# Kernel tuning notes

Measured on AMD Instinct MI355X. Metric: run time of the kernel, lower is better.

The kernel has to match this reference:

```python
import jax, jax.numpy as jnp
import numpy as np

H, W = 256, 256
FRONT_K = 8
ALPHA_T = 1.0 / 255.0
EPS = 1e-8               # transmittance early-stop threshold (meta_f32[4])
BG = (0.0, 0.0, 0.0)     # background color
CHUNK = 128              # gaussians composited per scan step


def setup_inputs() -> dict:
    key = jax.random.key(0)
    k1, k2, k3, k4, k5, k6, k7 = jax.random.split(key, 7)
    B, G = 2, 8192
    # gaussian centers spread over the image plane
    means2d = jax.random.uniform(k1, (B, G, 2), jnp.float32) * jnp.array([W, H], jnp.float32)
    # positive-definite conics (inverse 2D covariance): a, c > 0, |b| < sqrt(a*c)
    a = 0.05 + 0.45 * jax.random.uniform(k2, (B, G), jnp.float32)
    c = 0.05 + 0.45 * jax.random.uniform(k3, (B, G), jnp.float32)
    b = 0.5 * (jax.random.uniform(k4, (B, G), jnp.float32) - 0.5) * jnp.sqrt(a * c)
    conics = jnp.stack([a, b, c], axis=-1)
    colors = jax.random.uniform(k5, (B, G, 3), jnp.float32)
    opacities = jax.random.uniform(k6, (B, G), jnp.float32)
    depths = jax.random.uniform(k7, (B, G), jnp.float32) * 10.0
    return {"means2d": means2d, "conics": conics, "colors": colors,
            "opacities": opacities, "depths": depths}


def _rasterize_one(means2d, conics, colors, opacities, depths):
    # depth sort (stable, front-to-back)
    perm = jnp.argsort(depths, stable=True)
    m = means2d[perm]      # [G,2]
    co = conics[perm]      # [G,3]
    col = colors[perm]     # [G,3]
    op = opacities[perm]   # [G]
    G = m.shape[0]
    n_chunks = G // CHUNK

    px = jnp.arange(W, dtype=jnp.float32) + 0.5  # pixel centers
    py = jnp.arange(H, dtype=jnp.float32) + 0.5
    bg = jnp.asarray(BG, jnp.float32)

    def step(carry, chunk):
        accum, T, count = carry                    # [H,W,3], [H,W], [H,W] int32
        mC, coC, colC, opC = chunk                 # [K,2],[K,3],[K,3],[K]
        dx = px[None, None, :] - mC[:, 0][:, None, None]   # [K,1,W]
        dy = py[None, :, None] - mC[:, 1][:, None, None]   # [K,H,1]
        a = coC[:, 0][:, None, None]
        b = coC[:, 1][:, None, None]
        c = coC[:, 2][:, None, None]
        sigma = 0.5 * (a * dx * dx + c * dy * dy) + b * dx * dy  # [K,H,W]
        alpha = jnp.minimum(opC[:, None, None] * jnp.exp(-sigma), 0.999)
        alpha = jnp.where((sigma >= 0.0) & (alpha >= ALPHA_T), alpha, 0.0)
        kept = (alpha > 0.0).astype(jnp.int32)
        # front_k: only the first FRONT_K contributing gaussians per pixel
        before = count[None] + jnp.cumsum(kept, axis=0) - kept
        alpha = jnp.where(before < FRONT_K, alpha, 0.0)
        kept = (alpha > 0.0).astype(jnp.int32)
        one_m = 1.0 - alpha
        cp = jnp.cumprod(one_m, axis=0)                              # [K,H,W]
        Tc = T[None] * jnp.concatenate([jnp.ones((1, H, W), alpha.dtype), cp[:-1]], 0)
        w = jnp.where(Tc > EPS, Tc * alpha, 0.0)                     # early-stop gate
        accum = accum + jnp.einsum('khw,kc->hwc', w, colC)
        T = T * cp[-1]
        count = count + jnp.sum(kept, axis=0)
        return (accum, T, count), None

    chunks = (m.reshape(n_chunks, CHUNK, 2),
              co.reshape(n_chunks, CHUNK, 3),
              col.reshape(n_chunks, CHUNK, 3),
              op.reshape(n_chunks, CHUNK))
    init = (jnp.zeros((H, W, 3), jnp.float32),
            jnp.ones((H, W), jnp.float32),
            jnp.zeros((H, W), jnp.int32))
    (accum, T, _), _ = jax.lax.scan(step, init, chunks)
    return accum + T[..., None] * bg


def reference(means2d, conics, colors, opacities, depths):
    return jax.vmap(_rasterize_one)(means2d, conics, colors, opacities, depths)
```

## Files before the change

### kernel.cpp

```cpp
#include <hip/hip_runtime.h>
#include <math.h>

#define GN 8192
#define BN 2
#define HN 256
#define WN 256
#define FRONT_K 8
#define EPS_T 1e-8f
#define ALPHA_T (1.0f / 255.0f)
#define TDIM 32
#define NTILE (TDIM * TDIM)
#define CAP 256

__global__ __launch_bounds__(64) void pgr_clear(unsigned* __restrict__ cur)
{
    cur[blockIdx.x * 64 + threadIdx.x] = 0u;
}

__global__ __launch_bounds__(64) void pgr_prep(
    const float* __restrict__ means2d, const float* __restrict__ conics,
    const float* __restrict__ colors, const float* __restrict__ opac,
    const float* __restrict__ depths,
    float4* __restrict__ dat0, float4* __restrict__ dat1,
    float* __restrict__ dat2, unsigned long long* __restrict__ kdat,
    unsigned* __restrict__ cur, unsigned* __restrict__ ent)
{
    const int p = threadIdx.x >> 3;
    const int q = threadIdx.x & 7;
    int g = blockIdx.x * 8 + p;
    int b = g >> 13, i = g & (GN - 1);
    float2 mxy = reinterpret_cast<const float2*>(means2d)[g];
    float mx = mxy.x, my = mxy.y;
    float ca = conics[3 * g], cb = conics[3 * g + 1], cc = conics[3 * g + 2];
    float r = colors[3 * g], g2 = colors[3 * g + 1], b3 = colors[3 * g + 2];
    float op = opac[g];
    float dep = depths[g];

    if (q == 0) {
        dat0[g] = make_float4(mx, my, ca, cb);
        dat1[g] = make_float4(cc, op, r, g2);
        dat2[g] = b3;
        kdat[g] = ((unsigned long long)__float_as_uint(dep) << 13) | (unsigned)i;
    }

    float s = (op > 0.f) ? (__logf(255.0f * op) + 1e-4f) : -1.0f;
    if (s < 0.f) return;
    float det = fmaxf(ca * cc - cb * cb, 1e-12f);
    float dxm = sqrtf(2.f * s * cc / det) + 0.02f;
    float dym = sqrtf(2.f * s * ca / det) + 0.02f;
    int x0 = (int)floorf(mx - dxm - 0.5f), x1 = (int)ceilf(mx + dxm - 0.5f);
    int y0 = (int)floorf(my - dym - 0.5f), y1 = (int)ceilf(my + dym - 0.5f);
    if (x1 < 0 || x0 > WN - 1 || y1 < 0 || y0 > HN - 1) return;
    x0 = max(x0, 0); x1 = min(x1, WN - 1);
    y0 = max(y0, 0); y1 = min(y1, HN - 1);
    int tx0 = x0 >> 3, tx1 = x1 >> 3, ty0 = y0 >> 3, ty1 = y1 >> 3;
    int nx = tx1 - tx0 + 1;
    int ntl = nx * (ty1 - ty0 + 1);

    for (int idx = q; idx < ntl; idx += 8) {
        int ty = idx / nx;
        int tx = idx - ty * nx;
        int t = b * NTILE + (ty0 + ty) * TDIM + (tx0 + tx);
        unsigned pos = atomicAdd(&cur[t], 1u);
        if (pos < CAP) ent[t * CAP + (int)pos] = (unsigned)i;
    }
}

__device__ __forceinline__ int rank_of(const unsigned long long* s_key,
                                       unsigned long long k, int L)
{
    int rank = 0, j = 0;
    for (; j + 4 <= L; j += 4) {
        unsigned long long k0 = s_key[j], k1 = s_key[j + 1];
        unsigned long long k2 = s_key[j + 2], k3 = s_key[j + 3];
        rank += (int)(k0 < k) + (int)(k1 < k) + (int)(k2 < k) + (int)(k3 < k);
    }
    for (; j < L; ++j) rank += (int)(s_key[j] < k);
    return rank;
}

__global__ __launch_bounds__(256) void pgr_raster(
    const float4* __restrict__ dat0, const float4* __restrict__ dat1,
    const float* __restrict__ dat2, const unsigned long long* __restrict__ kdat,
    const unsigned* __restrict__ cur, const unsigned* __restrict__ ent,
    float* __restrict__ out)
{
    const int b = blockIdx.z;
    const int t = b * NTILE + blockIdx.y * TDIM + blockIdx.x;
    const int tid = threadIdx.x;
    const int tx0 = blockIdx.x * 8, ty0 = blockIdx.y * 8;
    const int bG = b * GN;

    __shared__ unsigned long long s_key[CAP];
    __shared__ float4 s_d0[CAP], s_d1[CAP];
    __shared__ float s_d2[CAP];

    const int base = t * CAP;
    const int L = min((int)cur[t], CAP);

    unsigned long long myk = 0;
    float4 r0, r1;
    float r2 = 0.f;
    if (tid < L) {
        int idx = bG + (int)ent[base + tid];
        myk = kdat[idx];
        r0 = dat0[idx];
        r1 = dat1[idx];
        r2 = dat2[idx];
        s_key[tid] = myk;
    }
    __syncthreads();

    if (tid < L) {
        int rank = rank_of(s_key, myk, L);
        s_d0[rank] = r0; s_d1[rank] = r1; s_d2[rank] = r2;
    }
    __syncthreads();

    if (tid >= 64) return;

    const int lx = tid & 7, ly = tid >> 3;
    const float px = tx0 + lx + 0.5f, py = ty0 + ly + 0.5f;

    float accR = 0.f, accG = 0.f, accB = 0.f, T = 1.f;
    int count = 0;
    bool done = false;

    for (int i0 = 0; i0 < L; i0 += 8) {
        if (__all((int)done)) break;
        float alpha[8], colR[8], colG[8], colB[8];
        bool valid[8];
        #pragma unroll
        for (int k = 0; k < 8; ++k) {
            int idx = i0 + k;
            bool act = (idx < L) && !done;
            int ii = act ? idx : i0;
            float4 d0 = s_d0[ii];
            float4 d1 = s_d1[ii];
            float dx = __fsub_rn(px, d0.x);
            float dy = __fsub_rn(py, d0.y);
            float t1 = __fmul_rn(__fmul_rn(d0.z, dx), dx);
            float t2 = __fmul_rn(__fmul_rn(d1.x, dy), dy);
            float sigma = __fadd_rn(__fmul_rn(0.5f, __fadd_rn(t1, t2)),
                                    __fmul_rn(__fmul_rn(d0.w, dx), dy));
            bool v = act && sigma >= 0.f && sigma <= 5.55f;
            float al = v ? fminf(__fmul_rn(d1.y, __expf(-sigma)), 0.999f) : 0.f;
            valid[k] = v && (al >= ALPHA_T);
            alpha[k] = al;
            colR[k] = d1.z; colG[k] = d1.w; colB[k] = s_d2[ii];
        }
        #pragma unroll
        for (int k = 0; k < 8; ++k) {
            if (valid[k] && !done) {
                float al = alpha[k];
                if (T > EPS_T) {
                    float w = __fmul_rn(T, al);
                    accR += w * colR[k];
                    accG += w * colG[k];
                    accB += w * colB[k];
                }
                T = __fmul_rn(T, __fsub_rn(1.f, al));
                count++;
                if (count >= FRONT_K || T <= EPS_T) done = true;
            }
        }
    }

    int o = ((b * HN + (ty0 + ly)) * WN + (tx0 + lx)) * 3;
    out[o] = accR;
    out[o + 1] = accG;
    out[o + 2] = accB;
}

extern "C" void kernel_launch(void* const* d_in, const int* in_sizes, int n_in,
                              void* d_out, int out_size, void* d_ws, size_t ws_size,
                              hipStream_t stream) {
    const float* means2d = (const float*)d_in[0];
    const float* conics  = (const float*)d_in[1];
    const float* colors  = (const float*)d_in[2];
    const float* opac    = (const float*)d_in[3];
    const float* depths  = (const float*)d_in[4];
    float* out = (float*)d_out;

    const int BG = BN * GN;
    float4*             dat0 = (float4*)d_ws;
    float4*             dat1 = dat0 + BG;
    float*              dat2 = (float*)(dat1 + BG);
    unsigned long long* kdat = (unsigned long long*)(dat2 + BG);
    unsigned*           cur  = (unsigned*)(kdat + BG);
    unsigned*           ent  = cur + BN * NTILE;

    pgr_clear<<<(BN * NTILE) / 64, 64, 0, stream>>>(cur);
    pgr_prep<<<(BN * GN) / 8, 64, 0, stream>>>(means2d, conics, colors, opac,
                                               depths, dat0, dat1, dat2, kdat,
                                               cur, ent);
    pgr_raster<<<dim3(TDIM, TDIM, BN), 256, 0, stream>>>(
        dat0, dat1, dat2, kdat, cur, ent, out);
}
```

Before: 39.13 us.

## Fuse binning and rasterization into one persistent kernel with grid barrier

Merges the prep/binning kernel and the raster kernel into a single launch of 512 blocks. The two phases are separated by a software grid-wide barrier built from an atomic counter with spin-wait. Each block now rasterizes four tiles, one per wavefront, each with its own shared-memory buffers. The per-wave sort loop is extended to handle lists longer than 64 entries. The aim is to remove a kernel launch boundary and its idle gap. The cost is a spin barrier that needs all 512 blocks co-resident, which risks deadlock if occupancy is insufficient, and four times the shared memory per block.

New measurement: 137.3 us. 251% more time.

```diff
diff --git a/kernel.cpp b/kernel.cpp
--- a/kernel.cpp
+++ b/kernel.cpp
@@ -11,59 +11,13 @@
 #define TDIM 32
 #define NTILE (TDIM * TDIM)
 #define CAP 256
+#define NBLK 512
+#define TPB 4
 
 __global__ __launch_bounds__(64) void pgr_clear(unsigned* __restrict__ cur)
 {
-    cur[blockIdx.x * 64 + threadIdx.x] = 0u;
-}
-
-__global__ __launch_bounds__(64) void pgr_prep(
-    const float* __restrict__ means2d, const float* __restrict__ conics,
-    const float* __restrict__ colors, const float* __restrict__ opac,
-    const float* __restrict__ depths,
-    float4* __restrict__ dat0, float4* __restrict__ dat1,
-    float* __restrict__ dat2, unsigned long long* __restrict__ kdat,
-    unsigned* __restrict__ cur, unsigned* __restrict__ ent)
-{
-    const int p = threadIdx.x >> 3;
-    const int q = threadIdx.x & 7;
-    int g = blockIdx.x * 8 + p;
-    int b = g >> 13, i = g & (GN - 1);
-    float2 mxy = reinterpret_cast<const float2*>(means2d)[g];
-    float mx = mxy.x, my = mxy.y;
-    float ca = conics[3 * g], cb = conics[3 * g + 1], cc = conics[3 * g + 2];
-    float r = colors[3 * g], g2 = colors[3 * g + 1], b3 = colors[3 * g + 2];
-    float op = opac[g];
-    float dep = depths[g];
-
-    if (q == 0) {
-        dat0[g] = make_float4(mx, my, ca, cb);
-        dat1[g] = make_float4(cc, op, r, g2);
-        dat2[g] = b3;
-        kdat[g] = ((unsigned long long)__float_as_uint(dep) << 13) | (unsigned)i;
-    }
-
-    float s = (op > 0.f) ? (__logf(255.0f * op) + 1e-4f) : -1.0f;
-    if (s < 0.f) return;
-    float det = fmaxf(ca * cc - cb * cb, 1e-12f);
-    float dxm = sqrtf(2.f * s * cc / det) + 0.02f;
-    float dym = sqrtf(2.f * s * ca / det) + 0.02f;
-    int x0 = (int)floorf(mx - dxm - 0.5f), x1 = (int)ceilf(mx + dxm - 0.5f);
-    int y0 = (int)floorf(my - dym - 0.5f), y1 = (int)ceilf(my + dym - 0.5f);
-    if (x1 < 0 || x0 > WN - 1 || y1 < 0 || y0 > HN - 1) return;
-    x0 = max(x0, 0); x1 = min(x1, WN - 1);
-    y0 = max(y0, 0); y1 = min(y1, HN - 1);
-    int tx0 = x0 >> 3, tx1 = x1 >> 3, ty0 = y0 >> 3, ty1 = y1 >> 3;
-    int nx = tx1 - tx0 + 1;
-    int ntl = nx * (ty1 - ty0 + 1);
-
-    for (int idx = q; idx < ntl; idx += 8) {
-        int ty = idx / nx;
-        int tx = idx - ty * nx;
-        int t = b * NTILE + (ty0 + ty) * TDIM + (tx0 + tx);
-        unsigned pos = atomicAdd(&cur[t], 1u);
-        if (pos < CAP) ent[t * CAP + (int)pos] = (unsigned)i;
-    }
+    int i = blockIdx.x * 64 + threadIdx.x;
+    if (i < BN * NTILE + 16) cur[i] = 0u;
 }
 
 __device__ __forceinline__ int rank_of(const unsigned long long* s_key,
@@ -79,48 +33,110 @@
     return rank;
 }
 
-__global__ __launch_bounds__(256) void pgr_raster(
-    const float4* __restrict__ dat0, const float4* __restrict__ dat1,
-    const float* __restrict__ dat2, const unsigned long long* __restrict__ kdat,
-    const unsigned* __restrict__ cur, const unsigned* __restrict__ ent,
-    float* __restrict__ out)
+__global__ __launch_bounds__(256, 2) void pgr_fused(
+    const float* __restrict__ means2d, const float* __restrict__ conics,
+    const float* __restrict__ colors, const float* __restrict__ opac,
+    const float* __restrict__ depths,
+    float4* __restrict__ dat0, float4* __restrict__ dat1,
+    float* __restrict__ dat2, unsigned long long* __restrict__ kdat,
+    unsigned* __restrict__ cur, unsigned* __restrict__ bar,
+    unsigned* __restrict__ ent, float* __restrict__ out)
 {
-    const int b = blockIdx.z;
-    const int t = b * NTILE + blockIdx.y * TDIM + blockIdx.x;
-    const int tid = threadIdx.x;
-    const int tx0 = blockIdx.x * 8, ty0 = blockIdx.y * 8;
+    const int tid = threadIdx.x, bid = blockIdx.x;
+
+    {
+        const int p = tid >> 3;
+        const int q = tid & 7;
+        int g = bid * 32 + p;
+        int b = g >> 13, i = g & (GN - 1);
+        float2 mxy = reinterpret_cast<const float2*>(means2d)[g];
+        float mx = mxy.x, my = mxy.y;
+        float ca = conics[3 * g], cb = conics[3 * g + 1], cc = conics[3 * g + 2];
+        float r = colors[3 * g], g2 = colors[3 * g + 1], b3 = colors[3 * g + 2];
+        float op = opac[g];
+        float dep = depths[g];
+
+        if (q == 0) {
+            dat0[g] = make_float4(mx, my, ca, cb);
+            dat1[g] = make_float4(cc, op, r, g2);
+            dat2[g] = b3;
+            kdat[g] = ((unsigned long long)__float_as_uint(dep) << 13) | (unsigned)i;
+        }
+
+        float s = (op > 0.f) ? (__logf(255.0f * op) + 1e-4f) : -1.0f;
+        if (s >= 0.f) {
+            float det = fmaxf(ca * cc - cb * cb, 1e-12f);
+            float dxm = sqrtf(2.f * s * cc / det) + 0.02f;
+            float dym = sqrtf(2.f * s * ca / det) + 0.02f;
+            int x0 = (int)floorf(mx - dxm - 0.5f), x1 = (int)ceilf(mx + dxm - 0.5f);
+            int y0 = (int)floorf(my - dym - 0.5f), y1 = (int)ceilf(my + dym - 0.5f);
+            if (!(x1 < 0 || x0 > WN - 1 || y1 < 0 || y0 > HN - 1)) {
+                x0 = max(x0, 0); x1 = min(x1, WN - 1);
+                y0 = max(y0, 0); y1 = min(y1, HN - 1);
+                int tx0 = x0 >> 3, ty0 = y0 >> 3;
+                int nx = (x1 >> 3) - tx0 + 1;
+                int ntl = nx * ((y1 >> 3) - ty0 + 1);
+                for (int idx = q; idx < ntl; idx += 8) {
+                    int ty = idx / nx;
+                    int tx = idx - ty * nx;
+                    int t = b * NTILE + (ty0 + ty) * TDIM + (tx0 + tx);
+                    unsigned pos = atomicAdd(&cur[t], 1u);
+                    if (pos < CAP) ent[t * CAP + (int)pos] = (unsigned)i;
+                }
+            }
+        }
+    }
+
+    __threadfence();
+    __syncthreads();
+    if (tid == 0) {
+        __hip_atomic_fetch_add(bar, 1u, __ATOMIC_ACQ_REL, __HIP_MEMORY_SCOPE_AGENT);
+        while (__hip_atomic_load(bar, __ATOMIC_ACQUIRE, __HIP_MEMORY_SCOPE_AGENT)
+               < (unsigned)NBLK)
+            __builtin_amdgcn_s_sleep(2);
+    }
+    __syncthreads();
+    __threadfence();
+
+    __shared__ unsigned long long s_key[TPB][CAP];
+    __shared__ float4 s_d0[TPB][CAP], s_d1[TPB][CAP];
+    __shared__ float s_d2[TPB][CAP];
+
+    const int w = tid >> 6, lane = tid & 63;
+    const int t = bid * TPB + w;
+    const int b = t >> 10;
+    const int rr = t & (NTILE - 1);
+    const int tx0 = (rr & (TDIM - 1)) * 8, ty0 = (rr >> 5) * 8;
+    const int lx = lane & 7, ly = lane >> 3;
+    const float px = tx0 + lx + 0.5f, py = ty0 + ly + 0.5f;
     const int bG = b * GN;
-
-    __shared__ unsigned long long s_key[CAP];
-    __shared__ float4 s_d0[CAP], s_d1[CAP];
-    __shared__ float s_d2[CAP];
-
     const int base = t * CAP;
     const int L = min((int)cur[t], CAP);
 
     unsigned long long myk = 0;
     float4 r0, r1;
     float r2 = 0.f;
-    if (tid < L) {
-        int idx = bG + (int)ent[base + tid];
+    if (lane < L) {
+        int idx = bG + (int)ent[base + lane];
         myk = kdat[idx];
-        r0 = dat0[idx];
-        r1 = dat1[idx];
-        r2 = dat2[idx];
-        s_key[tid] = myk;
-    }
-    __syncthreads();
-
-    if (tid < L) {
-        int rank = rank_of(s_key, myk, L);
-        s_d0[rank] = r0; s_d1[rank] = r1; s_d2[rank] = r2;
-    }
-    __syncthreads();
-
-    if (tid >= 64) return;
-
-    const int lx = tid & 7, ly = tid >> 3;
-    const float px = tx0 + lx + 0.5f, py = ty0 + ly + 0.5f;
+        r0 = dat0[idx]; r1 = dat1[idx]; r2 = dat2[idx];
+        s_key[w][lane] = myk;
+    }
+    for (int i = 64 + lane; i < L; i += 64)
+        s_key[w][i] = kdat[bG + (int)ent[base + i]];
+    __syncthreads();
+
+    if (lane < L) {
+        int rk = rank_of(s_key[w], myk, L);
+        s_d0[w][rk] = r0; s_d1[w][rk] = r1; s_d2[w][rk] = r2;
+    }
+    for (int i = 64 + lane; i < L; i += 64) {
+        unsigned long long k = s_key[w][i];
+        int rk = rank_of(s_key[w], k, L);
+        int idx = bG + (int)ent[base + i];
+        s_d0[w][rk] = dat0[idx]; s_d1[w][rk] = dat1[idx]; s_d2[w][rk] = dat2[idx];
+    }
+    __syncthreads();
 
     float accR = 0.f, accG = 0.f, accB = 0.f, T = 1.f;
     int count = 0;
@@ -135,8 +151,8 @@
             int idx = i0 + k;
             bool act = (idx < L) && !done;
             int ii = act ? idx : i0;
-            float4 d0 = s_d0[ii];
-            float4 d1 = s_d1[ii];
+            float4 d0 = s_d0[w][ii];
+            float4 d1 = s_d1[w][ii];
             float dx = __fsub_rn(px, d0.x);
             float dy = __fsub_rn(py, d0.y);
             float t1 = __fmul_rn(__fmul_rn(d0.z, dx), dx);
@@ -147,17 +163,17 @@
             float al = v ? fminf(__fmul_rn(d1.y, __expf(-sigma)), 0.999f) : 0.f;
             valid[k] = v && (al >= ALPHA_T);
             alpha[k] = al;
-            colR[k] = d1.z; colG[k] = d1.w; colB[k] = s_d2[ii];
+            colR[k] = d1.z; colG[k] = d1.w; colB[k] = s_d2[w][ii];
         }
         #pragma unroll
         for (int k = 0; k < 8; ++k) {
             if (valid[k] && !done) {
                 float al = alpha[k];
                 if (T > EPS_T) {
-                    float w = __fmul_rn(T, al);
-                    accR += w * colR[k];
-                    accG += w * colG[k];
-                    accB += w * colB[k];
+                    float wgt = __fmul_rn(T, al);
+                    accR += wgt * colR[k];
+                    accG += wgt * colG[k];
+                    accB += wgt * colB[k];
                 }
                 T = __fmul_rn(T, __fsub_rn(1.f, al));
                 count++;
@@ -188,12 +204,11 @@
     float*              dat2 = (float*)(dat1 + BG);
     unsigned long long* kdat = (unsigned long long*)(dat2 + BG);
     unsigned*           cur  = (unsigned*)(kdat + BG);
-    unsigned*           ent  = cur + BN * NTILE;
-
-    pgr_clear<<<(BN * NTILE) / 64, 64, 0, stream>>>(cur);
-    pgr_prep<<<(BN * GN) / 8, 64, 0, stream>>>(means2d, conics, colors, opac,
-                                               depths, dat0, dat1, dat2, kdat,
-                                               cur, ent);
-    pgr_raster<<<dim3(TDIM, TDIM, BN), 256, 0, stream>>>(
-        dat0, dat1, dat2, kdat, cur, ent, out);
-}
+    unsigned*           bar  = cur + BN * NTILE;
+    unsigned*           ent  = bar + 16;
+
+    pgr_clear<<<(BN * NTILE + 16 + 63) / 64, 64, 0, stream>>>(cur);
+    pgr_fused<<<NBLK, 256, 0, stream>>>(means2d, conics, colors, opac, depths,
+                                        dat0, dat1, dat2, kdat, cur, bar, ent,
+                                        out);
+}
```
